# Kernel optimization log

Hardware: AMD Instinct MI355X
Metric: run time of the kernel (lower is better)

The kernel has to match this reference:

```python
import jax, jax.numpy as jnp
import numpy as np

DIM = 128      # channels C
HEADS = 4
HD = DIM // HEADS  # head_dim = 32
N = 128        # window tokens = 2*8*8
BW = 2048      # B_ = batch * num_windows
NP = 256       # sp_mask partitions
NW = 256       # shift-mask windows
TABLE = 675    # (2*2-1)*(2*8-1)*(2*8-1)
SCALE = HD ** -0.5


def setup_inputs() -> dict:
    key = jax.random.key(0)
    ks = jax.random.split(key, 8)
    x = jax.random.normal(ks[0], (BW, N, DIM), jnp.float32)
    rpi = jax.random.randint(ks[1], (N, N), 0, TABLE, dtype=jnp.int32)
    mask = jax.random.normal(ks[2], (NW, N, N), jnp.float32)
    sp_mask = jax.random.normal(ks[3], (NP, N, N), jnp.float32)
    w_qkv = jax.random.normal(ks[4], (3 * DIM, DIM), jnp.float32) * 0.02
    b_qkv = jnp.zeros((3 * DIM,), jnp.float32)
    bias_table = jax.random.normal(ks[5], (TABLE, HEADS), jnp.float32) * 0.02
    w_proj = jax.random.normal(ks[6], (DIM, DIM), jnp.float32) * 0.02
    b_proj = jnp.zeros((DIM,), jnp.float32)
    return {"x": x, "rpi": rpi, "mask": mask, "sp_mask": sp_mask,
            "w_qkv": w_qkv, "b_qkv": b_qkv, "bias_table": bias_table,
            "w_proj": w_proj, "b_proj": b_proj}


def reference(x, rpi, mask, sp_mask, w_qkv, b_qkv, bias_table, w_proj, b_proj):
    B_, Nn, C = x.shape
    # qkv projection -> (B_, N, 3, H, hd)
    qkv = (x @ w_qkv.T + b_qkv).reshape(B_, Nn, 3, HEADS, HD)
    q = qkv[:, :, 0].transpose(0, 2, 1, 3) * SCALE  # (B_, H, N, hd)
    k = qkv[:, :, 1].transpose(0, 2, 1, 3)
    v = qkv[:, :, 2].transpose(0, 2, 1, 3)
    attn = jnp.einsum('bhnd,bhmd->bhnm', q, k)  # (B_, H, N, N)
    # gathered relative position bias: (N, N, H) -> (H, N, N)
    rpb = bias_table[rpi].transpose(2, 0, 1)
    attn = attn + rpb[None]
    # additive sparse mask, broadcast over B_//nP groups and heads
    attn = (attn.reshape(B_ // NP, NP, HEADS, Nn, Nn)
            + sp_mask[None, :, None]).reshape(B_, HEADS, Nn, Nn)
    # additive shift mask, broadcast over B_//nW groups and heads
    attn = (attn.reshape(B_ // NW, NW, HEADS, Nn, Nn)
            + mask[None, :, None]).reshape(B_, HEADS, Nn, Nn)
    attn = jax.nn.softmax(attn, axis=-1)
    out = jnp.einsum('bhnm,bhmd->bnhd', attn, v).reshape(B_, Nn, C)
    return out @ w_proj.T + b_proj
```

## Files before the change

kernel.cpp:

```cpp
#include <hip/hip_runtime.h>

typedef short v8s __attribute__((ext_vector_type(8)));
typedef float v4f __attribute__((ext_vector_type(4)));

#define MFMA16(a, b, c) __builtin_amdgcn_mfma_f32_16x16x32_bf16(a, b, c, 0, 0, 0)

__device__ __forceinline__ unsigned short f2b(float f) {
  union { float f; unsigned int i; } v;
  v.f = f;
  unsigned int x = v.i;
  return (unsigned short)((x + 0x7fffu + ((x >> 16) & 1u)) >> 16);
}
__device__ __forceinline__ v8s ldf8(const float* p) {
  float4 a = *(const float4*)p;
  float4 b = *(const float4*)(p + 4);
  union { v8s v; unsigned short u[8]; } r;
  r.u[0] = f2b(a.x); r.u[1] = f2b(a.y); r.u[2] = f2b(a.z); r.u[3] = f2b(a.w);
  r.u[4] = f2b(b.x); r.u[5] = f2b(b.y); r.u[6] = f2b(b.z); r.u[7] = f2b(b.w);
  return r.v;
}
__device__ __forceinline__ v8s ld16u(const unsigned short* p) {
  union { v8s v; ushort4 h[2]; } u;
  u.h[0] = *(const ushort4*)(p);
  u.h[1] = *(const ushort4*)(p + 4);
  return u.v;
}

#define SCALE 0.17677669529663687f
#define LOG2E 1.4426950408889634f
#define QSCALE (SCALE * LOG2E)

#define WS_RPB 16777216
#define WS_WQH 17039360
#define WS_WPH 17137664

__global__ __launch_bounds__(256)
void conv_w(const float* __restrict__ wq, const float* __restrict__ wp,
            unsigned short* __restrict__ wqh, unsigned short* __restrict__ wph) {
  int i = blockIdx.x * 256 + threadIdx.x;
  if (i < 384 * 128) wqh[i] = f2b(wq[i]);
  else wph[i - 384 * 128] = f2b(wp[i - 384 * 128]);
}

__global__ __launch_bounds__(256)
void build_bias(const float* __restrict__ mask, const float* __restrict__ sp,
                const int* __restrict__ rpi, const float* __restrict__ btab,
                float* __restrict__ msum, float* __restrict__ rpb) {
  const int wgrp = blockIdx.x, tid = threadIdx.x;
  const float* mk = mask + (size_t)wgrp * 16384;
  const float* sk = sp + (size_t)wgrp * 16384;
  float* ot = msum + (size_t)wgrp * 16384;
  for (int it = 0; it < 16; ++it) {
    int i = (tid + 256 * it) * 4;
    float4 a = *(const float4*)(mk + i);
    float4 b = *(const float4*)(sk + i);
    float4 s;
    s.x = (a.x + b.x) * LOG2E; s.y = (a.y + b.y) * LOG2E;
    s.z = (a.z + b.z) * LOG2E; s.w = (a.w + b.w) * LOG2E;
    *(float4*)(ot + i) = s;
  }
  int e = wgrp * 256 + tid;
  int hh = e >> 14, r = e & 16383;
  rpb[e] = btab[rpi[r] * 4 + hh] * LOG2E;
}

__global__ __launch_bounds__(256, 4)
void attn_kernel(const float* __restrict__ xg,
                 const unsigned short* __restrict__ wqh,
                 const float* __restrict__ bq,
                 const float* __restrict__ msum,
                 const float* __restrict__ rpb,
                 float* __restrict__ o_ws) {
  __shared__ alignas(16) unsigned char smem[17664];
  unsigned short* kss = (unsigned short*)smem;
  unsigned short* vs  = (unsigned short*)(smem + 9216);

  const int tid = threadIdx.x;
  const int wv = tid >> 6;
  const int lane = tid & 63;
  const int qd = lane >> 4;
  const int t16 = lane & 15;

  const int idx = blockIdx.x;
  const int wgrp = idx >> 5;
  const int rem = idx & 31;
  const int h = rem >> 3;
  const int b = (rem & 7) * 256 + wgrp;

  const float* xb = xg + (size_t)b * 16384;
  v8s bx[2][4];
  for (int nt = 0; nt < 2; ++nt)
    for (int ks = 0; ks < 4; ++ks) {
      int n = 32 * wv + nt * 16 + t16;
      bx[nt][ks] = ldf8(xb + n * 128 + ks * 32 + 8 * qd);
    }

  v4f accqk[4][2];
  for (int jt = 0; jt < 4; ++jt)
    for (int nt = 0; nt < 2; ++nt) accqk[jt][nt] = v4f{0.f, 0.f, 0.f, 0.f};
  for (int jt = 0; jt < 4; ++jt) {
    int wbase = (jt < 2) ? (h * 32 + jt * 16) : (128 + h * 32 + (jt - 2) * 16);
    for (int ks = 0; ks < 4; ++ks) {
      v8s a = *(const v8s*)(wqh + (wbase + t16) * 128 + ks * 32 + 8 * qd);
      for (int nt = 0; nt < 2; ++nt)
        accqk[jt][nt] = MFMA16(a, bx[nt][ks], accqk[jt][nt]);
    }
  }
  v4f accv[2][2];
  for (int rt = 0; rt < 2; ++rt)
    for (int ct = 0; ct < 2; ++ct) accv[rt][ct] = v4f{0.f, 0.f, 0.f, 0.f};
  for (int ct = 0; ct < 2; ++ct)
    for (int ks = 0; ks < 4; ++ks) {
      v8s bw = *(const v8s*)(wqh + (256 + h * 32 + ct * 16 + t16) * 128 + ks * 32 + 8 * qd);
      for (int rt = 0; rt < 2; ++rt)
        accv[rt][ct] = MFMA16(bx[rt][ks], bw, accv[rt][ct]);
    }

  for (int jt = 2; jt < 4; ++jt)
    for (int nt = 0; nt < 2; ++nt) {
      int n = 32 * wv + nt * 16 + t16;
      ushort4 pk;
      float v0 = accqk[jt][nt][0] + bq[128 + h * 32 + (jt - 2) * 16 + 4 * qd + 0];
      float v1 = accqk[jt][nt][1] + bq[128 + h * 32 + (jt - 2) * 16 + 4 * qd + 1];
      float v2 = accqk[jt][nt][2] + bq[128 + h * 32 + (jt - 2) * 16 + 4 * qd + 2];
      float v3 = accqk[jt][nt][3] + bq[128 + h * 32 + (jt - 2) * 16 + 4 * qd + 3];
      pk.x = f2b(v0); pk.y = f2b(v1); pk.z = f2b(v2); pk.w = f2b(v3);
      *(ushort4*)(kss + n * 36 + (jt - 2) * 16 + 4 * qd) = pk;
    }
  for (int ct = 0; ct < 2; ++ct) {
    int d = ct * 16 + t16;
    float bv = bq[256 + h * 32 + d];
    for (int rt = 0; rt < 2; ++rt) {
      ushort4 pk;
      pk.x = f2b(accv[rt][ct][0] + bv);
      pk.y = f2b(accv[rt][ct][1] + bv);
      pk.z = f2b(accv[rt][ct][2] + bv);
      pk.w = f2b(accv[rt][ct][3] + bv);
      *(ushort4*)(vs + d * 132 + 32 * wv + rt * 16 + 4 * qd) = pk;
    }
  }

  unsigned int qpk[2][2][2];
  for (int jt = 0; jt < 2; ++jt)
    for (int nt = 0; nt < 2; ++nt) {
      float vv[4];
      for (int r = 0; r < 4; ++r)
        vv[r] = (accqk[jt][nt][r] + bq[h * 32 + jt * 16 + 4 * qd + r]) * QSCALE;
      qpk[jt][nt][0] = (unsigned int)f2b(vv[0]) | ((unsigned int)f2b(vv[1]) << 16);
      qpk[jt][nt][1] = (unsigned int)f2b(vv[2]) | ((unsigned int)f2b(vv[3]) << 16);
    }
  const int srcA = ((qd & 1) << 5) + t16;
  const bool hiq = qd >= 2;
  v8s aq[2];
  for (int rt = 0; rt < 2; ++rt) {
    union { v8s v; unsigned int d[4]; } u;
    unsigned int a0 = __shfl((int)qpk[0][rt][0], srcA, 64);
    unsigned int b0 = __shfl((int)qpk[1][rt][0], srcA, 64);
    unsigned int a1 = __shfl((int)qpk[0][rt][1], srcA, 64);
    unsigned int b1 = __shfl((int)qpk[1][rt][1], srcA, 64);
    unsigned int a2 = __shfl((int)qpk[0][rt][0], srcA + 16, 64);
    unsigned int b2 = __shfl((int)qpk[1][rt][0], srcA + 16, 64);
    unsigned int a3 = __shfl((int)qpk[0][rt][1], srcA + 16, 64);
    unsigned int b3 = __shfl((int)qpk[1][rt][1], srcA + 16, 64);
    u.d[0] = hiq ? b0 : a0;
    u.d[1] = hiq ? b1 : a1;
    u.d[2] = hiq ? b2 : a2;
    u.d[3] = hiq ? b3 : a3;
    aq[rt] = u.v;
  }
  __syncthreads();

  v4f sa[2][8];
  const v4f zero4 = {0.f, 0.f, 0.f, 0.f};
  for (int ct = 0; ct < 8; ++ct) {
    v8s bk = ld16u(kss + (ct * 16 + t16) * 36 + 8 * qd);
    for (int nt = 0; nt < 2; ++nt)
      sa[nt][ct] = MFMA16(bk, aq[nt], zero4);
  }
  {
    const float* mt = msum + (size_t)wgrp * 16384;
    const float* rb = rpb + (size_t)h * 16384;
    for (int nt = 0; nt < 2; ++nt) {
      int n = 32 * wv + nt * 16 + t16;
      const float* pm = mt + n * 128;
      const float* pr = rb + n * 128;
      for (int ct = 0; ct < 8; ++ct) {
        float4 b1 = *(const float4*)(pm + ct * 16 + 4 * qd);
        float4 b2 = *(const float4*)(pr + ct * 16 + 4 * qd);
        sa[nt][ct][0] += b1.x + b2.x;
        sa[nt][ct][1] += b1.y + b2.y;
        sa[nt][ct][2] += b1.z + b2.z;
        sa[nt][ct][3] += b1.w + b2.w;
      }
    }
  }
  float pinv[2];
  for (int nt = 0; nt < 2; ++nt) {
    float m0 = sa[nt][0][0];
    for (int ct = 0; ct < 8; ++ct)
      for (int r = 0; r < 4; ++r) m0 = fmaxf(m0, sa[nt][ct][r]);
    m0 = fmaxf(m0, __shfl_xor(m0, 16));
    m0 = fmaxf(m0, __shfl_xor(m0, 32));
    for (int ct = 0; ct < 8; ++ct)
      for (int r = 0; r < 4; ++r)
        sa[nt][ct][r] = exp2f(sa[nt][ct][r] - m0);
    float s0 = 0.f;
    for (int ct = 0; ct < 8; ++ct)
      for (int r = 0; r < 4; ++r) s0 += sa[nt][ct][r];
    s0 += __shfl_xor(s0, 16);
    s0 += __shfl_xor(s0, 32);
    pinv[nt] = 1.0f / s0;
  }

  v8s av[2][4];
  for (int rt = 0; rt < 2; ++rt)
    for (int ks = 0; ks < 4; ++ks)
      av[rt][ks] = ld16u(vs + (rt * 16 + t16) * 132 + ks * 32 + 8 * qd);

  const int srcP0 = ((qd & 1) << 5) + t16;
  const bool hip2 = qd >= 2;
  for (int nt = 0; nt < 2; ++nt) {
    unsigned int pkd[8][2];
    for (int ct = 0; ct < 8; ++ct) {
      pkd[ct][0] = (unsigned int)f2b(sa[nt][ct][0]) | ((unsigned int)f2b(sa[nt][ct][1]) << 16);
      pkd[ct][1] = (unsigned int)f2b(sa[nt][ct][2]) | ((unsigned int)f2b(sa[nt][ct][3]) << 16);
    }
    v8s bp[4];
    for (int ks = 0; ks < 4; ++ks) {
      union { v8s v; unsigned int d[4]; } u;
      unsigned int a0 = __shfl((int)pkd[2 * ks][0], srcP0, 64);
      unsigned int b0 = __shfl((int)pkd[2 * ks + 1][0], srcP0, 64);
      unsigned int a1 = __shfl((int)pkd[2 * ks][1], srcP0, 64);
      unsigned int b1 = __shfl((int)pkd[2 * ks + 1][1], srcP0, 64);
      unsigned int a2 = __shfl((int)pkd[2 * ks][0], srcP0 + 16, 64);
      unsigned int b2 = __shfl((int)pkd[2 * ks + 1][0], srcP0 + 16, 64);
      unsigned int a3 = __shfl((int)pkd[2 * ks][1], srcP0 + 16, 64);
      unsigned int b3 = __shfl((int)pkd[2 * ks + 1][1], srcP0 + 16, 64);
      u.d[0] = hip2 ? b0 : a0;
      u.d[1] = hip2 ? b1 : a1;
      u.d[2] = hip2 ? b2 : a2;
      u.d[3] = hip2 ? b3 : a3;
      bp[ks] = u.v;
    }
    v4f oa[2] = {zero4, zero4};
    for (int ks = 0; ks < 4; ++ks)
      for (int rt = 0; rt < 2; ++rt)
        oa[rt] = MFMA16(av[rt][ks], bp[ks], oa[rt]);
    int n = 32 * wv + nt * 16 + t16;
    float s = pinv[nt];
    for (int rt = 0; rt < 2; ++rt) {
      int cbase = h * 32 + rt * 16 + 4 * qd;
      float4 pk;
      pk.x = oa[rt][0] * s;
      pk.y = oa[rt][1] * s;
      pk.z = oa[rt][2] * s;
      pk.w = oa[rt][3] * s;
      *(float4*)(o_ws + ((size_t)(b * 128 + n)) * 128 + cbase) = pk;
    }
  }
}

__global__ __launch_bounds__(256, 4)
void proj_kernel(const unsigned short* __restrict__ wph,
                 const float* __restrict__ bpj,
                 float* __restrict__ out) {
  const int tid = threadIdx.x;
  const int wv = tid >> 6;
  const int lane = tid & 63;
  const int qd = lane >> 4;
  const int t16 = lane & 15;
  const size_t row0 = (size_t)blockIdx.x * 128;
  const float* src = out + row0 * 128;

  v8s bo[2][4];
  for (int ct = 0; ct < 2; ++ct)
    for (int ks = 0; ks < 4; ++ks) {
      int n = 32 * wv + ct * 16 + t16;
      bo[ct][ks] = ldf8(src + n * 128 + ks * 32 + 8 * qd);
    }
  v4f acc[8][2];
  for (int rt = 0; rt < 8; ++rt)
    for (int ct = 0; ct < 2; ++ct) acc[rt][ct] = v4f{0.f, 0.f, 0.f, 0.f};
  for (int rt = 0; rt < 8; ++rt)
    for (int ks = 0; ks < 4; ++ks) {
      v8s a = *(const v8s*)(wph + (rt * 16 + t16) * 128 + ks * 32 + 8 * qd);
      for (int ct = 0; ct < 2; ++ct)
        acc[rt][ct] = MFMA16(a, bo[ct][ks], acc[rt][ct]);
    }
  for (int rt = 0; rt < 8; ++rt) {
    float4 bj = *(const float4*)(bpj + rt * 16 + 4 * qd);
    for (int ct = 0; ct < 2; ++ct) {
      int n = 32 * wv + ct * 16 + t16;
      float4 pk;
      pk.x = acc[rt][ct][0] + bj.x;
      pk.y = acc[rt][ct][1] + bj.y;
      pk.z = acc[rt][ct][2] + bj.z;
      pk.w = acc[rt][ct][3] + bj.w;
      *(float4*)(out + (row0 + n) * 128 + rt * 16 + 4 * qd) = pk;
    }
  }
}

extern "C" void kernel_launch(void* const* d_in, const int* in_sizes, int n_in,
                              void* d_out, int out_size, void* d_ws, size_t ws_size,
                              hipStream_t stream) {
  (void)in_sizes; (void)n_in; (void)out_size; (void)ws_size;
  const float* xg   = (const float*)d_in[0];
  const int*   rpi  = (const int*)d_in[1];
  const float* mask = (const float*)d_in[2];
  const float* sp   = (const float*)d_in[3];
  const float* wq   = (const float*)d_in[4];
  const float* bq   = (const float*)d_in[5];
  const float* btab = (const float*)d_in[6];
  const float* wp   = (const float*)d_in[7];
  const float* bpj  = (const float*)d_in[8];
  float* out = (float*)d_out;

  float* msum = (float*)d_ws;
  float* rpb  = (float*)((char*)d_ws + WS_RPB);
  unsigned short* wqh = (unsigned short*)((char*)d_ws + WS_WQH);
  unsigned short* wph = (unsigned short*)((char*)d_ws + WS_WPH);

  conv_w<<<256, 256, 0, stream>>>(wq, wp, wqh, wph);
  build_bias<<<256, 256, 0, stream>>>(mask, sp, rpi, btab, msum, rpb);
  attn_kernel<<<8192, 256, 0, stream>>>(xg, wqh, bq, msum, rpb, out);
  proj_kernel<<<2048, 256, 0, stream>>>(wph, bpj, out);
}
```

Before: 553.0 us.

## Pre-convert x to bf16, store attention output as bf16, use packed cvt

Adds a pre-pass that converts x to bf16 once, so each of the four per-head attention blocks reads half the bytes and skips the per-element rounding. The attention output is written as bf16 into workspace instead of fp32, which halves that intermediate traffic and the projection kernel's reads. Manual float-to-bf16 rounding is replaced by the hardware v_cvt_pk_bf16_f32 instruction, and the LDS row padding changes so that K and V can be read with single 16-byte loads. Which paths run depends on workspace size. The extra pass costs a full read and write of x, and the bf16 intermediate adds rounding error.

```diff
diff --git a/kernel.cpp b/kernel.cpp
--- a/kernel.cpp
+++ b/kernel.cpp
@@ -11,28 +11,31 @@
   unsigned int x = v.i;
   return (unsigned short)((x + 0x7fffu + ((x >> 16) & 1u)) >> 16);
 }
+__device__ __forceinline__ unsigned int cvtpk(float lo, float hi) {
+  unsigned int r;
+  asm("v_cvt_pk_bf16_f32 %0, %1, %2" : "=v"(r) : "v"(lo), "v"(hi));
+  return r;
+}
 __device__ __forceinline__ v8s ldf8(const float* p) {
   float4 a = *(const float4*)p;
   float4 b = *(const float4*)(p + 4);
-  union { v8s v; unsigned short u[8]; } r;
-  r.u[0] = f2b(a.x); r.u[1] = f2b(a.y); r.u[2] = f2b(a.z); r.u[3] = f2b(a.w);
-  r.u[4] = f2b(b.x); r.u[5] = f2b(b.y); r.u[6] = f2b(b.z); r.u[7] = f2b(b.w);
+  union { v8s v; unsigned int d[4]; } r;
+  r.d[0] = cvtpk(a.x, a.y); r.d[1] = cvtpk(a.z, a.w);
+  r.d[2] = cvtpk(b.x, b.y); r.d[3] = cvtpk(b.z, b.w);
   return r.v;
-}
-__device__ __forceinline__ v8s ld16u(const unsigned short* p) {
-  union { v8s v; ushort4 h[2]; } u;
-  u.h[0] = *(const ushort4*)(p);
-  u.h[1] = *(const ushort4*)(p + 4);
-  return u.v;
 }
 
 #define SCALE 0.17677669529663687f
 #define LOG2E 1.4426950408889634f
 #define QSCALE (SCALE * LOG2E)
 
-#define WS_RPB 16777216
-#define WS_WQH 17039360
-#define WS_WPH 17137664
+#define WS_RPB   16777216
+#define WS_WQH   17039360
+#define WS_WPH   17137664
+#define WS_OH    17170432
+#define WS_XH    84279296
+#define WS_END_OBF 84279296ull
+#define WS_END_XH  151388160ull
 
 __global__ __launch_bounds__(256)
 void conv_w(const float* __restrict__ wq, const float* __restrict__ wp,
@@ -64,16 +67,30 @@
   rpb[e] = btab[rpi[r] * 4 + hh] * LOG2E;
 }
 
+__global__ __launch_bounds__(256)
+void build_xh(const float* __restrict__ x, unsigned short* __restrict__ xh) {
+  size_t i = ((size_t)blockIdx.x * 256 + threadIdx.x) * 8;
+  float4 a = *(const float4*)(x + i);
+  float4 b = *(const float4*)(x + i + 4);
+  union { int4 v; unsigned int d[4]; } pk;
+  pk.d[0] = cvtpk(a.x, a.y); pk.d[1] = cvtpk(a.z, a.w);
+  pk.d[2] = cvtpk(b.x, b.y); pk.d[3] = cvtpk(b.z, b.w);
+  *(int4*)(xh + i) = pk.v;
+}
+
+template <bool XH, bool OBF>
 __global__ __launch_bounds__(256, 4)
 void attn_kernel(const float* __restrict__ xg,
+                 const unsigned short* __restrict__ xhg,
                  const unsigned short* __restrict__ wqh,
                  const float* __restrict__ bq,
                  const float* __restrict__ msum,
                  const float* __restrict__ rpb,
-                 float* __restrict__ o_ws) {
-  __shared__ alignas(16) unsigned char smem[17664];
+                 float* __restrict__ o32,
+                 unsigned short* __restrict__ o16) {
+  __shared__ alignas(16) unsigned char smem[18944];
   unsigned short* kss = (unsigned short*)smem;
-  unsigned short* vs  = (unsigned short*)(smem + 9216);
+  unsigned short* vs  = (unsigned short*)(smem + 10240);
 
   const int tid = threadIdx.x;
   const int wv = tid >> 6;
@@ -87,13 +104,22 @@
   const int h = rem >> 3;
   const int b = (rem & 7) * 256 + wgrp;
 
-  const float* xb = xg + (size_t)b * 16384;
   v8s bx[2][4];
-  for (int nt = 0; nt < 2; ++nt)
-    for (int ks = 0; ks < 4; ++ks) {
-      int n = 32 * wv + nt * 16 + t16;
-      bx[nt][ks] = ldf8(xb + n * 128 + ks * 32 + 8 * qd);
-    }
+  if constexpr (XH) {
+    const unsigned short* xb = xhg + (size_t)b * 16384;
+    for (int nt = 0; nt < 2; ++nt)
+      for (int ks = 0; ks < 4; ++ks) {
+        int n = 32 * wv + nt * 16 + t16;
+        bx[nt][ks] = *(const v8s*)(xb + n * 128 + ks * 32 + 8 * qd);
+      }
+  } else {
+    const float* xb = xg + (size_t)b * 16384;
+    for (int nt = 0; nt < 2; ++nt)
+      for (int ks = 0; ks < 4; ++ks) {
+        int n = 32 * wv + nt * 16 + t16;
+        bx[nt][ks] = ldf8(xb + n * 128 + ks * 32 + 8 * qd);
+      }
+  }
 
   v4f accqk[4][2];
   for (int jt = 0; jt < 4; ++jt)
@@ -119,35 +145,33 @@
   for (int jt = 2; jt < 4; ++jt)
     for (int nt = 0; nt < 2; ++nt) {
       int n = 32 * wv + nt * 16 + t16;
-      ushort4 pk;
-      float v0 = accqk[jt][nt][0] + bq[128 + h * 32 + (jt - 2) * 16 + 4 * qd + 0];
-      float v1 = accqk[jt][nt][1] + bq[128 + h * 32 + (jt - 2) * 16 + 4 * qd + 1];
-      float v2 = accqk[jt][nt][2] + bq[128 + h * 32 + (jt - 2) * 16 + 4 * qd + 2];
-      float v3 = accqk[jt][nt][3] + bq[128 + h * 32 + (jt - 2) * 16 + 4 * qd + 3];
-      pk.x = f2b(v0); pk.y = f2b(v1); pk.z = f2b(v2); pk.w = f2b(v3);
-      *(ushort4*)(kss + n * 36 + (jt - 2) * 16 + 4 * qd) = pk;
+      int bb = 128 + h * 32 + (jt - 2) * 16 + 4 * qd;
+      uint2 pk;
+      pk.x = cvtpk(accqk[jt][nt][0] + bq[bb + 0], accqk[jt][nt][1] + bq[bb + 1]);
+      pk.y = cvtpk(accqk[jt][nt][2] + bq[bb + 2], accqk[jt][nt][3] + bq[bb + 3]);
+      *(uint2*)(kss + n * 40 + (jt - 2) * 16 + 4 * qd) = pk;
     }
   for (int ct = 0; ct < 2; ++ct) {
     int d = ct * 16 + t16;
     float bv = bq[256 + h * 32 + d];
     for (int rt = 0; rt < 2; ++rt) {
-      ushort4 pk;
-      pk.x = f2b(accv[rt][ct][0] + bv);
-      pk.y = f2b(accv[rt][ct][1] + bv);
-      pk.z = f2b(accv[rt][ct][2] + bv);
-      pk.w = f2b(accv[rt][ct][3] + bv);
-      *(ushort4*)(vs + d * 132 + 32 * wv + rt * 16 + 4 * qd) = pk;
+      uint2 pk;
+      pk.x = cvtpk(accv[rt][ct][0] + bv, accv[rt][ct][1] + bv);
+      pk.y = cvtpk(accv[rt][ct][2] + bv, accv[rt][ct][3] + bv);
+      *(uint2*)(vs + d * 136 + 32 * wv + rt * 16 + 4 * qd) = pk;
     }
   }
 
   unsigned int qpk[2][2][2];
   for (int jt = 0; jt < 2; ++jt)
     for (int nt = 0; nt < 2; ++nt) {
-      float vv[4];
-      for (int r = 0; r < 4; ++r)
-        vv[r] = (accqk[jt][nt][r] + bq[h * 32 + jt * 16 + 4 * qd + r]) * QSCALE;
-      qpk[jt][nt][0] = (unsigned int)f2b(vv[0]) | ((unsigned int)f2b(vv[1]) << 16);
-      qpk[jt][nt][1] = (unsigned int)f2b(vv[2]) | ((unsigned int)f2b(vv[3]) << 16);
+      int bb = h * 32 + jt * 16 + 4 * qd;
+      float v0 = (accqk[jt][nt][0] + bq[bb + 0]) * QSCALE;
+      float v1 = (accqk[jt][nt][1] + bq[bb + 1]) * QSCALE;
+      float v2 = (accqk[jt][nt][2] + bq[bb + 2]) * QSCALE;
+      float v3 = (accqk[jt][nt][3] + bq[bb + 3]) * QSCALE;
+      qpk[jt][nt][0] = cvtpk(v0, v1);
+      qpk[jt][nt][1] = cvtpk(v2, v3);
     }
   const int srcA = ((qd & 1) << 5) + t16;
   const bool hiq = qd >= 2;
@@ -173,7 +197,7 @@
   v4f sa[2][8];
   const v4f zero4 = {0.f, 0.f, 0.f, 0.f};
   for (int ct = 0; ct < 8; ++ct) {
-    v8s bk = ld16u(kss + (ct * 16 + t16) * 36 + 8 * qd);
+    v8s bk = *(const v8s*)(kss + (ct * 16 + t16) * 40 + 8 * qd);
     for (int nt = 0; nt < 2; ++nt)
       sa[nt][ct] = MFMA16(bk, aq[nt], zero4);
   }
@@ -215,15 +239,15 @@
   v8s av[2][4];
   for (int rt = 0; rt < 2; ++rt)
     for (int ks = 0; ks < 4; ++ks)
-      av[rt][ks] = ld16u(vs + (rt * 16 + t16) * 132 + ks * 32 + 8 * qd);
+      av[rt][ks] = *(const v8s*)(vs + (rt * 16 + t16) * 136 + ks * 32 + 8 * qd);
 
   const int srcP0 = ((qd & 1) << 5) + t16;
   const bool hip2 = qd >= 2;
   for (int nt = 0; nt < 2; ++nt) {
     unsigned int pkd[8][2];
     for (int ct = 0; ct < 8; ++ct) {
-      pkd[ct][0] = (unsigned int)f2b(sa[nt][ct][0]) | ((unsigned int)f2b(sa[nt][ct][1]) << 16);
-      pkd[ct][1] = (unsigned int)f2b(sa[nt][ct][2]) | ((unsigned int)f2b(sa[nt][ct][3]) << 16);
+      pkd[ct][0] = cvtpk(sa[nt][ct][0], sa[nt][ct][1]);
+      pkd[ct][1] = cvtpk(sa[nt][ct][2], sa[nt][ct][3]);
     }
     v8s bp[4];
     for (int ks = 0; ks < 4; ++ks) {
@@ -248,36 +272,55 @@
         oa[rt] = MFMA16(av[rt][ks], bp[ks], oa[rt]);
     int n = 32 * wv + nt * 16 + t16;
     float s = pinv[nt];
-    for (int rt = 0; rt < 2; ++rt) {
-      int cbase = h * 32 + rt * 16 + 4 * qd;
-      float4 pk;
-      pk.x = oa[rt][0] * s;
-      pk.y = oa[rt][1] * s;
-      pk.z = oa[rt][2] * s;
-      pk.w = oa[rt][3] * s;
-      *(float4*)(o_ws + ((size_t)(b * 128 + n)) * 128 + cbase) = pk;
-    }
-  }
-}
-
+    if constexpr (OBF) {
+      for (int rt = 0; rt < 2; ++rt) {
+        uint2 pk;
+        pk.x = cvtpk(oa[rt][0] * s, oa[rt][1] * s);
+        pk.y = cvtpk(oa[rt][2] * s, oa[rt][3] * s);
+        *(uint2*)(o16 + ((size_t)(b * 128 + n)) * 128 + h * 32 + rt * 16 + 4 * qd) = pk;
+      }
+    } else {
+      for (int rt = 0; rt < 2; ++rt) {
+        float4 pk;
+        pk.x = oa[rt][0] * s;
+        pk.y = oa[rt][1] * s;
+        pk.z = oa[rt][2] * s;
+        pk.w = oa[rt][3] * s;
+        *(float4*)(o32 + ((size_t)(b * 128 + n)) * 128 + h * 32 + rt * 16 + 4 * qd) = pk;
+      }
+    }
+  }
+}
+
+template <bool OBF>
 __global__ __launch_bounds__(256, 4)
 void proj_kernel(const unsigned short* __restrict__ wph,
                  const float* __restrict__ bpj,
-                 float* __restrict__ out) {
+                 const unsigned short* __restrict__ o16,
+                 float* out) {
   const int tid = threadIdx.x;
   const int wv = tid >> 6;
   const int lane = tid & 63;
   const int qd = lane >> 4;
   const int t16 = lane & 15;
   const size_t row0 = (size_t)blockIdx.x * 128;
-  const float* src = out + row0 * 128;
 
   v8s bo[2][4];
-  for (int ct = 0; ct < 2; ++ct)
-    for (int ks = 0; ks < 4; ++ks) {
-      int n = 32 * wv + ct * 16 + t16;
-      bo[ct][ks] = ldf8(src + n * 128 + ks * 32 + 8 * qd);
-    }
+  if constexpr (OBF) {
+    const unsigned short* src = o16 + row0 * 128;
+    for (int ct = 0; ct < 2; ++ct)
+      for (int ks = 0; ks < 4; ++ks) {
+        int n = 32 * wv + ct * 16 + t16;
+        bo[ct][ks] = *(const v8s*)(src + n * 128 + ks * 32 + 8 * qd);
+      }
+  } else {
+    const float* src = out + row0 * 128;
+    for (int ct = 0; ct < 2; ++ct)
+      for (int ks = 0; ks < 4; ++ks) {
+        int n = 32 * wv + ct * 16 + t16;
+        bo[ct][ks] = ldf8(src + n * 128 + ks * 32 + 8 * qd);
+      }
+  }
   v4f acc[8][2];
   for (int rt = 0; rt < 8; ++rt)
     for (int ct = 0; ct < 2; ++ct) acc[rt][ct] = v4f{0.f, 0.f, 0.f, 0.f};
@@ -304,7 +347,7 @@
 extern "C" void kernel_launch(void* const* d_in, const int* in_sizes, int n_in,
                               void* d_out, int out_size, void* d_ws, size_t ws_size,
                               hipStream_t stream) {
-  (void)in_sizes; (void)n_in; (void)out_size; (void)ws_size;
+  (void)in_sizes; (void)n_in; (void)out_size;
   const float* xg   = (const float*)d_in[0];
   const int*   rpi  = (const int*)d_in[1];
   const float* mask = (const float*)d_in[2];
@@ -320,9 +363,22 @@
   float* rpb  = (float*)((char*)d_ws + WS_RPB);
   unsigned short* wqh = (unsigned short*)((char*)d_ws + WS_WQH);
   unsigned short* wph = (unsigned short*)((char*)d_ws + WS_WPH);
+  unsigned short* oh  = (unsigned short*)((char*)d_ws + WS_OH);
+  unsigned short* xh  = (unsigned short*)((char*)d_ws + WS_XH);
+
+  const bool obf = ws_size >= WS_END_OBF;
+  const bool xhp = ws_size >= WS_END_XH;
 
   conv_w<<<256, 256, 0, stream>>>(wq, wp, wqh, wph);
   build_bias<<<256, 256, 0, stream>>>(mask, sp, rpi, btab, msum, rpb);
-  attn_kernel<<<8192, 256, 0, stream>>>(xg, wqh, bq, msum, rpb, out);
-  proj_kernel<<<2048, 256, 0, stream>>>(wph, bpj, out);
-}
+  if (xhp) {
+    build_xh<<<16384, 256, 0, stream>>>(xg, xh);
+    attn_kernel<true, true><<<8192, 256, 0, stream>>>(xg, xh, wqh, bq, msum, rpb, out, oh);
+  } else if (obf) {
+    attn_kernel<false, true><<<8192, 256, 0, stream>>>(xg, xh, wqh, bq, msum, rpb, out, oh);
+  } else {
+    attn_kernel<false, false><<<8192, 256, 0, stream>>>(xg, xh, wqh, bq, msum, rpb, out, oh);
+  }
+  if (obf) proj_kernel<true><<<2048, 256, 0, stream>>>(wph, bpj, oh, out);
+  else     proj_kernel<false><<<2048, 256, 0, stream>>>(wph, bpj, oh, out);
+}
```

Result: no change. 560.5 us (+1.4%).
